# Optimization experiments

Hardware: AMD Instinct MI355X
Metric: run time of the kernel (lower is better)

The kernel has to match this reference:

```python
import jax, jax.numpy as jnp
import numpy as np
import math

B, T, O, C, H, L, V, S = 4, 1024, 128, 1024, 16, 4, 32000, 4096
D = C // H
PAD = 0


def setup_inputs() -> dict:
    key = jax.random.key(0)
    ks = jax.random.split(key, 16)
    r = lambda i, shape, s=0.02: jax.random.normal(ks[i], shape, jnp.float32) * s
    return {
        "tokens_w": jax.random.randint(ks[0], (B, T), 0, V).astype(jnp.int32),
        "pos_offset": 0,
        "mem": jax.random.normal(ks[1], (B, O, C), jnp.float32),
        "ssum": jax.random.normal(ks[2], (B, C), jnp.float32),
        "tok_emb_w": r(3, (V, C)),
        "pos_emb_w": r(4, (S, C)),
        "mem_w": r(5, (C, C)), "mem_b": jnp.zeros((C,), jnp.float32),
        "memln_s": jnp.ones((C,), jnp.float32), "memln_b": jnp.zeros((C,), jnp.float32),
        "alpha_p": jnp.zeros((C,), jnp.float32),
        "sum_w": r(6, (C, C)),
        "ln1_s": jnp.ones((L, C), jnp.float32), "ln1_b": jnp.zeros((L, C), jnp.float32),
        "Wq": r(7, (L, C, C)), "bq": jnp.zeros((L, C), jnp.float32),
        "Wk": r(8, (L, C, C)), "bk": jnp.zeros((L, C), jnp.float32),
        "Wv": r(9, (L, C, C)), "bv": jnp.zeros((L, C), jnp.float32),
        "Wo": r(10, (L, C, C)), "bo": jnp.zeros((L, C), jnp.float32),
        "ln2_s": jnp.ones((L, C), jnp.float32), "ln2_b": jnp.zeros((L, C), jnp.float32),
        "W1": r(11, (L, C, 4 * C)), "b1": jnp.zeros((L, 4 * C), jnp.float32),
        "W2": r(12, (L, 4 * C, C)), "b2": jnp.zeros((L, C), jnp.float32),
        "fln_s": jnp.ones((C,), jnp.float32), "fln_b": jnp.zeros((C,), jnp.float32),
        "head_w": r(13, (C, V)), "head_b": jnp.zeros((V,), jnp.float32),
        "lam_p": jnp.zeros((C,), jnp.float32),
    }


def _ln(x, s, b, eps=1e-6):
    mu = jnp.mean(x, -1, keepdims=True)
    var = jnp.mean((x - mu) ** 2, -1, keepdims=True)
    return (x - mu) * jax.lax.rsqrt(var + eps) * s + b


def reference(tokens_w, pos_offset, mem, ssum, tok_emb_w, pos_emb_w, mem_w, mem_b,
              memln_s, memln_b, alpha_p, sum_w, ln1_s, ln1_b, Wq, bq, Wk, bk, Wv, bv,
              Wo, bo, ln2_s, ln2_b, W1, b1, W2, b2, fln_s, fln_b, head_w, head_b, lam_p):
    Bx, Tx = tokens_w.shape
    tok = tok_emb_w[tokens_w]                                   # [B,T,C]
    pos_ids = jnp.clip(jnp.arange(Tx, dtype=jnp.int32) + pos_offset, 0, S - 1)
    x = tok + pos_emb_w[pos_ids][None, :, :]
    # memory adapter + norm (saved-before-masking memory state)
    m2 = _ln(mem @ mem_w + mem_b, memln_s, memln_b)             # [B,O,C]
    alpha = jax.nn.sigmoid(alpha_p)
    x = x + ((ssum @ sum_w) * alpha[None, :])[:, None, :]
    # boolean mask: memory tokens always visible + causal window + key padding
    causal = jnp.concatenate([jnp.ones((Tx, O), bool),
                              jnp.tril(jnp.ones((Tx, Tx), bool))], axis=1)[None, None]
    key_ok = jnp.concatenate([jnp.ones((Bx, O), bool), tokens_w != PAD], axis=1)
    mask = causal & key_ok[:, None, None, :]                    # [B,1,T,O+T]
    scale = 1.0 / math.sqrt(D)
    for i in range(L):
        kv = jnp.concatenate([m2, x], axis=1)                   # [B,O+T,C]
        h = _ln(x, ln1_s[i], ln1_b[i])
        q = (h @ Wq[i] + bq[i]).reshape(Bx, Tx, H, D)
        k = (kv @ Wk[i] + bk[i]).reshape(Bx, O + Tx, H, D)
        v = (kv @ Wv[i] + bv[i]).reshape(Bx, O + Tx, H, D)
        att = jnp.einsum('bqhd,bkhd->bhqk', q, k) * scale
        att = jnp.where(mask, att, -1e9)
        p = jax.nn.softmax(att, axis=-1)
        o = jnp.einsum('bhqk,bkhd->bqhd', p, v).reshape(Bx, Tx, C)
        x = x + (o @ Wo[i] + bo[i])
        h = _ln(x, ln2_s[i], ln2_b[i])
        x = x + (jax.nn.gelu(h @ W1[i] + b1[i]) @ W2[i] + b2[i])
    x = _ln(x, fln_s, fln_b)
    new_mem = x[:, -O:, :]
    m = (tokens_w != PAD).astype(x.dtype)
    x = x * m[:, :, None]
    logits = x @ head_w + head_b                                # [B,T,V]
    summary = jnp.sum(x * m[:, :, None], axis=1) / (jnp.sum(m, axis=1, keepdims=True) + 1e-6)
    lam = jax.nn.sigmoid(lam_p)
    new_ssum = ssum * lam[None, :] + summary * (1.0 - lam[None, :])
    return (new_mem, new_ssum, logits)
```

## Files before the change

### kernel.cpp

```cpp
#include <hip/hip_runtime.h>
#include <hip/hip_bf16.h>

typedef __bf16 bf16_t;
typedef __bf16 bf16x8 __attribute__((ext_vector_type(8)));
typedef __bf16 bf16x4 __attribute__((ext_vector_type(4)));
typedef float f32x4 __attribute__((ext_vector_type(4)));

#define NB 4
#define NT 1024
#define NO 128
#define NC 1024
#define NH 16
#define NL 4
#define NV 32000
#define NS 4096
#define ND 64
#define NTK (NO + NT)

#define GLOAD_LDS16(g, l) __builtin_amdgcn_global_load_lds( \
    (__attribute__((address_space(1))) void*)(g), \
    (__attribute__((address_space(3))) void*)(l), 16, 0, 0)

__device__ __forceinline__ float sigmoidf_(float x) { return 1.0f / (1.0f + __expf(-x)); }

template<int EPI>
__global__ __launch_bounds__(512) void gemm8p(
    const bf16_t* __restrict__ A, const bf16_t* __restrict__ Bt,
    const float* __restrict__ bias, float* __restrict__ outF,
    bf16_t* __restrict__ outB, int M, int N, int K, int ldo, int gm)
{
    __shared__ bf16_t sm[65536];
    const int tid = threadIdx.x;
    const int w = tid >> 6, lane = tid & 63;
    const int wr = w >> 2, wc = w & 3;
    const int lr = lane & 15, lk = lane >> 4;
    const int nwg = gridDim.x;
    const int bid = blockIdx.x;
    const int xcd = bid & 7, base = bid >> 3;
    const int qq = nwg >> 3, rr = nwg & 7;
    int wg = (xcd < rr ? xcd * (qq + 1) : rr * (qq + 1) + (xcd - rr) * qq) + base;
    const int nnt = N >> 8;
    const int gsz = gm * nnt;
    const int g = wg / gsz, r2 = wg - g * gsz;
    const int ntl = r2 / gm, mt = g * gm + (r2 - ntl * gm);
    const int bm = mt << 8, bn = ntl << 8;
    const bf16_t* Ab = A + (size_t)bm * K;
    const bf16_t* Bb = Bt + (size_t)bn * K;
    const int srow = tid >> 3;
    const int scol = ((tid & 7) ^ (srow & 7)) << 3;
    const int nk = K >> 6;
    f32x4 acc[8][4] = {};

    auto STAGE = [&](int b, int kt, int h) {
        const bf16_t* gsrc = (h < 2) ? Ab : Bb;
        const int half = h & 1;
        char* lbase = (char*)(sm + ((h < 2) ? 0 : 32768) + b * 16384 + half * 8192);
        #pragma unroll
        for (int i = 0; i < 2; ++i) {
            GLOAD_LDS16(gsrc + (size_t)(half * 128 + i * 64 + srow) * K + kt * 64 + scol,
                        lbase + (i * 512 + tid) * 16);
        }
    };

    #pragma unroll
    for (int h = 0; h < 4; ++h) STAGE(0, 0, h);
    asm volatile("s_waitcnt vmcnt(0)" ::: "memory");
    __builtin_amdgcn_s_barrier();

    for (int kt = 0; kt < nk; ++kt) {
        const int curb = kt & 1;
        const bool dostage = (kt + 1) < nk;
        const char* Abase = (const char*)(sm + curb * 16384);
        const char* Bbase = (const char*)(sm + 32768 + curb * 16384);

        if (dostage) {
            STAGE(curb ^ 1, kt + 1, 0);
            STAGE(curb ^ 1, kt + 1, 1);
            asm volatile("s_waitcnt vmcnt(4)" ::: "memory");
        } else {
            asm volatile("s_waitcnt vmcnt(0)" ::: "memory");
        }
        __builtin_amdgcn_s_barrier();

        bf16x8 bfr[4][2];
        #pragma unroll
        for (int n = 0; n < 4; ++n)
            #pragma unroll
            for (int ks = 0; ks < 2; ++ks) {
                const int row = wc * 64 + n * 16 + lr;
                bfr[n][ks] = *(const bf16x8*)(Bbase + row * 128 + ((((ks << 2) + lk) ^ (row & 7)) << 4));
            }
        bf16x8 af[4][2];
        #pragma unroll
        for (int m = 0; m < 4; ++m)
            #pragma unroll
            for (int ks = 0; ks < 2; ++ks) {
                const int row = wr * 128 + m * 16 + lr;
                af[m][ks] = *(const bf16x8*)(Abase + row * 128 + ((((ks << 2) + lk) ^ (row & 7)) << 4));
            }
        asm volatile("s_waitcnt lgkmcnt(0)" ::: "memory");
        __builtin_amdgcn_sched_barrier(0);
        __builtin_amdgcn_s_setprio(1);
        #pragma unroll
        for (int m = 0; m < 4; ++m)
            #pragma unroll
            for (int n = 0; n < 4; ++n)
                #pragma unroll
                for (int ks = 0; ks < 2; ++ks)
                    acc[m][n] = __builtin_amdgcn_mfma_f32_16x16x32_bf16(
                        af[m][ks], bfr[n][ks], acc[m][n], 0, 0, 0);
        __builtin_amdgcn_s_setprio(0);

        if (dostage) {
            STAGE(curb ^ 1, kt + 1, 2);
            STAGE(curb ^ 1, kt + 1, 3);
        }
        bf16x8 ag[4][2];
        #pragma unroll
        for (int m = 0; m < 4; ++m)
            #pragma unroll
            for (int ks = 0; ks < 2; ++ks) {
                const int row = wr * 128 + 64 + m * 16 + lr;
                ag[m][ks] = *(const bf16x8*)(Abase + row * 128 + ((((ks << 2) + lk) ^ (row & 7)) << 4));
            }
        asm volatile("s_waitcnt lgkmcnt(0)" ::: "memory");
        __builtin_amdgcn_sched_barrier(0);
        __builtin_amdgcn_s_setprio(1);
        #pragma unroll
        for (int m = 0; m < 4; ++m)
            #pragma unroll
            for (int n = 0; n < 4; ++n)
                #pragma unroll
                for (int ks = 0; ks < 2; ++ks)
                    acc[4 + m][n] = __builtin_amdgcn_mfma_f32_16x16x32_bf16(
                        ag[m][ks], bfr[n][ks], acc[4 + m][n], 0, 0, 0);
        __builtin_amdgcn_s_setprio(0);
        __builtin_amdgcn_s_barrier();
    }

    float bv4[4];
    #pragma unroll
    for (int n = 0; n < 4; ++n) bv4[n] = bias[bn + wc * 64 + n * 16 + lr];
    #pragma unroll
    for (int m = 0; m < 8; ++m) {
        #pragma unroll
        for (int j = 0; j < 4; ++j) {
            const int row = bm + wr * 128 + m * 16 + lk * 4 + j;
            #pragma unroll
            for (int n = 0; n < 4; ++n) {
                const int col = bn + wc * 64 + n * 16 + lr;
                float v = acc[m][n][j] + bv4[n];
                if constexpr (EPI == 0) {
                    __builtin_nontemporal_store(v, &outF[(size_t)row * ldo + col]);
                } else {
                    float u = 1.5957691216057308f * (v + 0.044715f * v * v * v);
                    float g_ = v / (1.0f + __expf(-u));
                    outB[(size_t)row * ldo + col] = (bf16_t)g_;
                }
            }
        }
    }
}

#define EPI_F32  0
#define EPI_ADD  1
#define EPI_GELU 2
#define EPI_QKV  3
#define EPI_KV   4

template<int EPI>
__global__ __launch_bounds__(256) void gemm_bt(
    const bf16_t* __restrict__ A, const bf16_t* __restrict__ Bt,
    const float* __restrict__ bias, const float* __restrict__ bias2,
    float* __restrict__ outF, bf16_t* __restrict__ outB, bf16_t* __restrict__ outB2,
    int M, int N, int K, int p0, int ldo, int gm)
{
    __shared__ bf16_t lA[128 * 32];
    __shared__ bf16_t lB[128 * 32];
    const int tid = threadIdx.x;
    const int nwg = gridDim.x;
    const int bid = blockIdx.x;
    const int xcd = bid & 7, base = bid >> 3;
    const int qq = nwg >> 3, rr = nwg & 7;
    int wg = (xcd < rr ? xcd * (qq + 1) : rr * (qq + 1) + (xcd - rr) * qq) + base;
    const int nnt = N >> 7;
    const int gsz = gm * nnt;
    const int g = wg / gsz, r2 = wg - g * gsz;
    const int ntl = r2 / gm, mt = g * gm + (r2 - ntl * gm);
    const int bm = mt * 128, bn = ntl * 128;
    const bf16_t* Ab = A + (size_t)bm * K;
    const bf16_t* Bb = Bt + (size_t)bn * K;
    const int wave = tid >> 6, lane = tid & 63;
    const int wr = wave >> 1, wc = wave & 1;
    const int lr = lane & 15, lk = lane >> 4;
    f32x4 acc[4][4] = {};
    const int nk = K >> 5;
    const int c1 = tid, c2 = tid + 256;
    for (int kt = 0; kt < nk; ++kt) {
        __syncthreads();
        const bf16_t* Abk = Ab + kt * 32;
        const bf16_t* Bbk = Bb + kt * 32;
        GLOAD_LDS16(Abk + (size_t)(c1 >> 2) * K + (c1 & 3) * 8, (char*)lA + c1 * 16);
        GLOAD_LDS16(Abk + (size_t)(c2 >> 2) * K + (c2 & 3) * 8, (char*)lA + c2 * 16);
        GLOAD_LDS16(Bbk + (size_t)(c1 >> 2) * K + (c1 & 3) * 8, (char*)lB + c1 * 16);
        GLOAD_LDS16(Bbk + (size_t)(c2 >> 2) * K + (c2 & 3) * 8, (char*)lB + c2 * 16);
        __syncthreads();
        bf16x8 af[4], bfr[4];
        #pragma unroll
        for (int m = 0; m < 4; ++m)
            af[m] = *(const bf16x8*)&lA[(wr * 64 + m * 16 + lr) * 32 + lk * 8];
        #pragma unroll
        for (int n = 0; n < 4; ++n)
            bfr[n] = *(const bf16x8*)&lB[(wc * 64 + n * 16 + lr) * 32 + lk * 8];
        #pragma unroll
        for (int m = 0; m < 4; ++m)
            #pragma unroll
            for (int n = 0; n < 4; ++n)
                acc[m][n] = __builtin_amdgcn_mfma_f32_16x16x32_bf16(af[m], bfr[n], acc[m][n], 0, 0, 0);
    }
    #pragma unroll
    for (int m = 0; m < 4; ++m) {
        #pragma unroll
        for (int j = 0; j < 4; ++j) {
            const int row = bm + wr * 64 + m * 16 + lk * 4 + j;
            int b_ = 0, t_ = 0;
            if constexpr (EPI == EPI_QKV || EPI == EPI_KV) { b_ = row / p0; t_ = row % p0; }
            #pragma unroll
            for (int n = 0; n < 4; ++n) {
                const int col = bn + wc * 64 + n * 16 + lr;
                if constexpr (EPI == EPI_F32) {
                    float v = acc[m][n][j] + bias[col];
                    __builtin_nontemporal_store(v, &outF[(size_t)row * ldo + col]);
                } else if constexpr (EPI == EPI_ADD) {
                    float v = acc[m][n][j] + bias[col];
                    outF[(size_t)row * ldo + col] += v;
                } else if constexpr (EPI == EPI_GELU) {
                    float v = acc[m][n][j] + bias[col];
                    float u = 1.5957691216057308f * (v + 0.044715f * v * v * v);
                    float g_ = v / (1.0f + __expf(-u));
                    outB[(size_t)row * ldo + col] = (bf16_t)g_;
                } else if constexpr (EPI == EPI_QKV) {
                    float v = acc[m][n][j] + bias[col];
                    int h = col >> 6, d = col & 63;
                    outB[(((size_t)b_ * NH + h) * p0 + t_) * ND + d] = (bf16_t)v;
                } else if constexpr (EPI == EPI_KV) {
                    if (col < NC) {
                        float v = acc[m][n][j] + bias[col];
                        int h = col >> 6, d = col & 63;
                        outB[(((size_t)b_ * NH + h) * NTK + t_) * ND + d] = (bf16_t)v;
                    } else {
                        int c2_ = col - NC;
                        float v = acc[m][n][j] + bias2[c2_];
                        int h = c2_ >> 6, d = c2_ & 63;
                        outB2[(((size_t)b_ * NH + h) * ND + d) * NTK + t_] = (bf16_t)v;
                    }
                }
            }
        }
    }
}

__device__ __forceinline__ void tc_body(
    const float* __restrict__ W, bf16_t* __restrict__ Wt,
    int K, int N, int k0, int n0, int t)
{
    __shared__ float tile[64][65];
    #pragma unroll
    for (int i = 0; i < 4; ++i) {
        const int idx = t + i * 256;
        const int r = idx >> 4, c4 = (idx & 15) << 2;
        const float4 v = *(const float4*)(W + (size_t)(k0 + r) * N + n0 + c4);
        tile[r][c4 + 0] = v.x; tile[r][c4 + 1] = v.y;
        tile[r][c4 + 2] = v.z; tile[r][c4 + 3] = v.w;
    }
    __syncthreads();
    #pragma unroll
    for (int i = 0; i < 4; ++i) {
        const int idx = t + i * 256;
        const int r = idx >> 4, c4 = (idx & 15) << 2;
        bf16x4 o = {(bf16_t)tile[c4 + 0][r], (bf16_t)tile[c4 + 1][r],
                    (bf16_t)tile[c4 + 2][r], (bf16_t)tile[c4 + 3][r]};
        *(bf16x4*)(Wt + (size_t)(n0 + r) * K + k0 + c4) = o;
    }
}

__global__ __launch_bounds__(256) void transpose_cast(
    const float* __restrict__ W, bf16_t* __restrict__ Wt, int K, int N)
{
    tc_body(W, Wt, K, N, blockIdx.x << 6, blockIdx.y << 6, threadIdx.x);
}

__global__ __launch_bounds__(256) void transpose_layer(
    const float* __restrict__ Wq, const float* __restrict__ Wk,
    const float* __restrict__ Wv, const float* __restrict__ Wo,
    const float* __restrict__ W1, const float* __restrict__ W2,
    bf16_t* __restrict__ wtq, bf16_t* __restrict__ wtkv,
    bf16_t* __restrict__ wto, bf16_t* __restrict__ wt1, bf16_t* __restrict__ wt2)
{
    const int bid = blockIdx.x;
    const float* W; bf16_t* Wt; int K, N, k0, n0;
    if (bid < 1024) {
        const int which = bid >> 8, r = bid & 255;
        K = NC; N = NC;
        k0 = (r & 15) << 6; n0 = (r >> 4) << 6;
        W  = (which == 0) ? Wq : (which == 1) ? Wk : (which == 2) ? Wv : Wo;
        Wt = (which == 0) ? wtq : (which == 1) ? wtkv
           : (which == 2) ? (wtkv + (size_t)NC * NC) : wto;
    } else if (bid < 2048) {
        const int r = bid - 1024;
        K = NC; N = 4 * NC;
        k0 = (r & 15) << 6; n0 = (r >> 4) << 6;
        W = W1; Wt = wt1;
    } else {
        const int r = bid - 2048;
        K = 4 * NC; N = NC;
        k0 = (r & 63) << 6; n0 = (r >> 6) << 6;
        W = W2; Wt = wt2;
    }
    tc_body(W, Wt, K, N, k0, n0, threadIdx.x);
}

template<int MODE>
__global__ __launch_bounds__(256) void ln_row(
    const float* __restrict__ X, const float* __restrict__ sw,
    const float* __restrict__ bw, float* __restrict__ outF,
    bf16_t* __restrict__ outB, bf16_t* __restrict__ outB2)
{
    const int row = blockIdx.x;
    const int t = threadIdx.x;
    const float4 v = ((const float4*)(X + (size_t)row * NC))[t];
    float s1 = v.x + v.y + v.z + v.w;
    float s2 = v.x * v.x + v.y * v.y + v.z * v.z + v.w * v.w;
    #pragma unroll
    for (int off = 32; off > 0; off >>= 1) { s1 += __shfl_xor(s1, off); s2 += __shfl_xor(s2, off); }
    __shared__ float rs1[4], rs2[4];
    if ((t & 63) == 0) { rs1[t >> 6] = s1; rs2[t >> 6] = s2; }
    __syncthreads();
    s1 = rs1[0] + rs1[1] + rs1[2] + rs1[3];
    s2 = rs2[0] + rs2[1] + rs2[2] + rs2[3];
    const float mu = s1 * (1.0f / NC);
    const float var = s2 * (1.0f / NC) - mu * mu;
    const float rstd = rsqrtf(var + 1e-6f);
    const int c = t * 4;
    const float4 sv = ((const float4*)sw)[t];
    const float4 bv = ((const float4*)bw)[t];
    float y0 = (v.x - mu) * rstd * sv.x + bv.x;
    float y1 = (v.y - mu) * rstd * sv.y + bv.y;
    float y2 = (v.z - mu) * rstd * sv.z + bv.z;
    float y3 = (v.w - mu) * rstd * sv.w + bv.w;
    size_t dst;
    if constexpr (MODE == 1) dst = ((size_t)(row / NO) * NTK + (row % NO)) * NC + c;
    else dst = (size_t)row * NC + c;
    bf16x4 o = {(bf16_t)y0, (bf16_t)y1, (bf16_t)y2, (bf16_t)y3};
    *(bf16x4*)(outB + dst) = o;
    if constexpr (MODE == 3) {
        const int b_ = row >> 10, t_ = row & 1023;
        bf16x4 o2 = {(bf16_t)v.x, (bf16_t)v.y, (bf16_t)v.z, (bf16_t)v.w};
        *(bf16x4*)(outB2 + ((size_t)b_ * NTK + NO + t_) * NC + c) = o2;
    }
}

__global__ __launch_bounds__(256) void ln_final(
    const float* __restrict__ X, const float* __restrict__ sw,
    const float* __restrict__ bw, const int* __restrict__ tokens,
    bf16_t* __restrict__ xm, float* __restrict__ outMem)
{
    const int row = blockIdx.x;
    const int t = threadIdx.x;
    const float4 v = ((const float4*)(X + (size_t)row * NC))[t];
    float s1 = v.x + v.y + v.z + v.w;
    float s2 = v.x * v.x + v.y * v.y + v.z * v.z + v.w * v.w;
    #pragma unroll
    for (int off = 32; off > 0; off >>= 1) { s1 += __shfl_xor(s1, off); s2 += __shfl_xor(s2, off); }
    __shared__ float rs1[4], rs2[4];
    if ((t & 63) == 0) { rs1[t >> 6] = s1; rs2[t >> 6] = s2; }
    __syncthreads();
    s1 = rs1[0] + rs1[1] + rs1[2] + rs1[3];
    s2 = rs2[0] + rs2[1] + rs2[2] + rs2[3];
    const float mu = s1 * (1.0f / NC);
    const float var = s2 * (1.0f / NC) - mu * mu;
    const float rstd = rsqrtf(var + 1e-6f);
    const int c = t * 4;
    const float4 sv = ((const float4*)sw)[t];
    const float4 bv = ((const float4*)bw)[t];
    float y0 = (v.x - mu) * rstd * sv.x + bv.x;
    float y1 = (v.y - mu) * rstd * sv.y + bv.y;
    float y2 = (v.z - mu) * rstd * sv.z + bv.z;
    float y3 = (v.w - mu) * rstd * sv.w + bv.w;
    const bool ok = tokens[row] != 0;
    bf16x4 o;
    if (ok) { o = (bf16x4){(bf16_t)y0, (bf16_t)y1, (bf16_t)y2, (bf16_t)y3}; }
    else    { o = (bf16x4){(bf16_t)0.f, (bf16_t)0.f, (bf16_t)0.f, (bf16_t)0.f}; }
    *(bf16x4*)(xm + (size_t)row * NC + c) = o;
    const int b_ = row >> 10, t_ = row & 1023;
    if (t_ >= NT - NO) {
        float4 f; f.x = y0; f.y = y1; f.z = y2; f.w = y3;
        *(float4*)(outMem + ((size_t)b_ * NO + (t_ - (NT - NO))) * NC + c) = f;
    }
}

__global__ __launch_bounds__(256) void attn_kernel(
    const bf16_t* __restrict__ Q, const bf16_t* __restrict__ Kb,
    const bf16_t* __restrict__ Vt, const int* __restrict__ tokens,
    bf16_t* __restrict__ Ob)
{
    const int bh = blockIdx.x;
    const int b = bh >> 4, h = bh & 15;
    const int w = threadIdx.x >> 6;
    const int lane = threadIdx.x & 63;
    const int yt = gridDim.y - 1 - blockIdx.y;
    const int q0 = (yt << 6) + (w << 4);
    const int lr = lane & 15, lk = lane >> 4;
    const bf16_t* Qp = Q + ((size_t)bh * NT + q0) * ND;
    const bf16x8 qf0 = *(const bf16x8*)(Qp + lr * ND + lk * 8);
    const bf16x8 qf1 = *(const bf16x8*)(Qp + lr * ND + 32 + lk * 8);
    const bf16_t* Kbase = Kb + (size_t)bh * NTK * ND;
    const bf16_t* Vbase = Vt + (size_t)bh * ND * NTK;
    const int* tokb = tokens + b * NT;
    float mrow[4] = {-1e30f, -1e30f, -1e30f, -1e30f};
    float lsum[4] = {0.f, 0.f, 0.f, 0.f};
    f32x4 acc[4] = {};
    __shared__ bf16_t pb[4][16 * 64];
    char* pbw = (char*)pb[w];
    const int kmax = NO + q0 + 16;
    for (int k0 = 0; k0 < kmax; k0 += 64) {
        f32x4 st[4] = {};
        __builtin_amdgcn_s_setprio(1);
        #pragma unroll
        for (int nt = 0; nt < 4; ++nt) {
            const bf16_t* Kp = Kbase + (size_t)(k0 + nt * 16 + lr) * ND + lk * 8;
            bf16x8 kf0 = *(const bf16x8*)(Kp);
            bf16x8 kf1 = *(const bf16x8*)(Kp + 32);
            st[nt] = __builtin_amdgcn_mfma_f32_16x16x32_bf16(qf0, kf0, st[nt], 0, 0, 0);
            st[nt] = __builtin_amdgcn_mfma_f32_16x16x32_bf16(qf1, kf1, st[nt], 0, 0, 0);
        }
        __builtin_amdgcn_s_setprio(0);
        float sc[4][4];
        float tmax[4] = {-1e30f, -1e30f, -1e30f, -1e30f};
        #pragma unroll
        for (int nt = 0; nt < 4; ++nt) {
            const int key = k0 + nt * 16 + lr;
            const int kt = key - NO;
            const int kts = kt < 0 ? 0 : kt;
            const bool keyok = (kt < 0) | (tokb[kts] != 0);
            #pragma unroll
            for (int j = 0; j < 4; ++j) {
                const int qrow = q0 + lk * 4 + j;
                const bool ok = keyok && (kt <= qrow);
                const float s = ok ? st[nt][j] * 0.125f : -1e9f;
                sc[nt][j] = s;
                tmax[j] = fmaxf(tmax[j], s);
            }
        }
        #pragma unroll
        for (int off = 1; off < 16; off <<= 1)
            #pragma unroll
            for (int j = 0; j < 4; ++j) tmax[j] = fmaxf(tmax[j], __shfl_xor(tmax[j], off));
        float resc[4], p[4][4], psum[4] = {0.f, 0.f, 0.f, 0.f};
        #pragma unroll
        for (int j = 0; j < 4; ++j) {
            const float mnew = fmaxf(mrow[j], tmax[j]);
            resc[j] = __expf(mrow[j] - mnew);
            mrow[j] = mnew;
        }
        #pragma unroll
        for (int nt = 0; nt < 4; ++nt)
            #pragma unroll
            for (int j = 0; j < 4; ++j) { p[nt][j] = __expf(sc[nt][j] - mrow[j]); psum[j] += p[nt][j]; }
        #pragma unroll
        for (int off = 1; off < 16; off <<= 1)
            #pragma unroll
            for (int j = 0; j < 4; ++j) psum[j] += __shfl_xor(psum[j], off);
        #pragma unroll
        for (int j = 0; j < 4; ++j) lsum[j] = lsum[j] * resc[j] + psum[j];
        #pragma unroll
        for (int dt = 0; dt < 4; ++dt)
            #pragma unroll
            for (int j = 0; j < 4; ++j) acc[dt][j] *= resc[j];
        #pragma unroll
        for (int nt = 0; nt < 4; ++nt)
            #pragma unroll
            for (int j = 0; j < 4; ++j) {
                const int row = lk * 4 + j;
                const int byt = (row << 7) + ((((nt << 4) + lr) << 1) ^ ((row & 7) << 4));
                *(bf16_t*)(pbw + byt) = (bf16_t)p[nt][j];
            }
        const int swz = (lr & 7) << 4;
        const bf16x8 pa0 = *(const bf16x8*)(pbw + ((lr << 7) + (((lk << 4)) ^ swz)));
        const bf16x8 pa1 = *(const bf16x8*)(pbw + ((lr << 7) + ((64 + (lk << 4)) ^ swz)));
        __builtin_amdgcn_s_setprio(1);
        #pragma unroll
        for (int dt = 0; dt < 4; ++dt) {
            const bf16_t* Vp = Vbase + (size_t)(dt * 16 + lr) * NTK + k0 + lk * 8;
            bf16x8 vf0 = *(const bf16x8*)(Vp);
            bf16x8 vf1 = *(const bf16x8*)(Vp + 32);
            acc[dt] = __builtin_amdgcn_mfma_f32_16x16x32_bf16(pa0, vf0, acc[dt], 0, 0, 0);
            acc[dt] = __builtin_amdgcn_mfma_f32_16x16x32_bf16(pa1, vf1, acc[dt], 0, 0, 0);
        }
        __builtin_amdgcn_s_setprio(0);
    }
    #pragma unroll
    for (int dt = 0; dt < 4; ++dt)
        #pragma unroll
        for (int j = 0; j < 4; ++j)
            Ob[((size_t)b * NT + q0 + lk * 4 + j) * NC + h * ND + dt * 16 + lr] =
                (bf16_t)(acc[dt][j] / lsum[j]);
}

__global__ __launch_bounds__(256) void sum_proj_kernel(
    const float* __restrict__ ssum, const float* __restrict__ sumw,
    const float* __restrict__ alpha, float* __restrict__ add)
{
    const int b = blockIdx.y;
    const int c = blockIdx.x * 256 + threadIdx.x;
    float a = 0.f;
    for (int k = 0; k < NC; ++k) a += ssum[b * NC + k] * sumw[(size_t)k * NC + c];
    add[b * NC + c] = a * sigmoidf_(alpha[c]);
}

__global__ __launch_bounds__(256) void embed_kernel(
    const int* __restrict__ tokens, const int* __restrict__ posoff,
    const float* __restrict__ tokw, const float* __restrict__ posw,
    const float* __restrict__ add, float* __restrict__ X)
{
    const int bt = blockIdx.x;
    const int b = bt >> 10, t = bt & 1023;
    const int c = threadIdx.x * 4;
    const int tok = tokens[bt];
    int p = t + posoff[0];
    p = p < 0 ? 0 : (p > NS - 1 ? NS - 1 : p);
    const float4 tv = *(const float4*)(tokw + (size_t)tok * NC + c);
    const float4 pv = *(const float4*)(posw + (size_t)p * NC + c);
    const float4 av = *(const float4*)(add + b * NC + c);
    float4 o;
    o.x = tv.x + pv.x + av.x; o.y = tv.y + pv.y + av.y;
    o.z = tv.z + pv.z + av.z; o.w = tv.w + pv.w + av.w;
    *(float4*)(X + (size_t)bt * NC + c) = o;
}

__global__ __launch_bounds__(256) void cast_f32_bf16_kernel(
    const float* __restrict__ in, bf16_t* __restrict__ out)
{
    const size_t i = ((size_t)blockIdx.x * 256 + threadIdx.x) * 4;
    const float4 v = *(const float4*)(in + i);
    bf16x4 o = {(bf16_t)v.x, (bf16_t)v.y, (bf16_t)v.z, (bf16_t)v.w};
    *(bf16x4*)(out + i) = o;
}

__global__ __launch_bounds__(256) void sumpart_kernel(
    const bf16_t* __restrict__ XM, float* __restrict__ sbuf)
{
    const int b = blockIdx.z;
    const int c = blockIdx.x * 256 + threadIdx.x;
    const int t0 = blockIdx.y * 64;
    float a = 0.f;
    for (int t = t0; t < t0 + 64; ++t)
        a += (float)XM[((size_t)b * NT + t) * NC + c];
    atomicAdd(&sbuf[b * NC + c], a);
}

__global__ __launch_bounds__(256) void ssum_out_kernel(
    const float* __restrict__ sbuf, const int* __restrict__ tokens,
    const float* __restrict__ ssum, const float* __restrict__ lamp, float* __restrict__ out)
{
    const int b = blockIdx.y;
    const int c = blockIdx.x * 256 + threadIdx.x;
    int cnt = 0;
    for (int t = 0; t < NT; ++t) cnt += (tokens[b * NT + t] != 0);
    const float summary = sbuf[b * NC + c] / ((float)cnt + 1e-6f);
    const float lam = sigmoidf_(lamp[c]);
    out[b * NC + c] = ssum[b * NC + c] * lam + summary * (1.0f - lam);
}

extern "C" void kernel_launch(void* const* d_in, const int* in_sizes, int n_in,
                              void* d_out, int out_size, void* d_ws, size_t ws_size,
                              hipStream_t stream)
{
    (void)in_sizes; (void)n_in; (void)out_size; (void)ws_size;
    const int*   tokens   = (const int*)d_in[0];
    const int*   posoff   = (const int*)d_in[1];
    const float* mem      = (const float*)d_in[2];
    const float* ssum     = (const float*)d_in[3];
    const float* tok_emb  = (const float*)d_in[4];
    const float* pos_emb  = (const float*)d_in[5];
    const float* mem_w    = (const float*)d_in[6];
    const float* mem_b    = (const float*)d_in[7];
    const float* memln_s  = (const float*)d_in[8];
    const float* memln_b  = (const float*)d_in[9];
    const float* alpha_p  = (const float*)d_in[10];
    const float* sum_w    = (const float*)d_in[11];
    const float* ln1_s    = (const float*)d_in[12];
    const float* ln1_b    = (const float*)d_in[13];
    const float* Wq       = (const float*)d_in[14];
    const float* bq       = (const float*)d_in[15];
    const float* Wk       = (const float*)d_in[16];
    const float* bk       = (const float*)d_in[17];
    const float* Wv       = (const float*)d_in[18];
    const float* bv       = (const float*)d_in[19];
    const float* Wo       = (const float*)d_in[20];
    const float* bo       = (const float*)d_in[21];
    const float* ln2_s    = (const float*)d_in[22];
    const float* ln2_b    = (const float*)d_in[23];
    const float* W1       = (const float*)d_in[24];
    const float* b1       = (const float*)d_in[25];
    const float* W2       = (const float*)d_in[26];
    const float* b2       = (const float*)d_in[27];
    const float* fln_s    = (const float*)d_in[28];
    const float* fln_b    = (const float*)d_in[29];
    const float* head_w   = (const float*)d_in[30];
    const float* head_b   = (const float*)d_in[31];
    const float* lam_p    = (const float*)d_in[32];

    float* out_mem    = (float*)d_out;
    float* out_ssum   = out_mem + (size_t)NB * NO * NC;
    float* out_logits = out_ssum + (size_t)NB * NC;

    char* wp = (char*)d_ws;
    auto alloc = [&](size_t bytes) { char* p = wp; wp += (bytes + 255) & ~(size_t)255; return p; };
    bf16_t* wt_head = (bf16_t*)alloc((size_t)NV * NC * 2);
    bf16_t* wt_mem  = (bf16_t*)alloc((size_t)NC * NC * 2);
    bf16_t* wt_q    = (bf16_t*)alloc((size_t)NC * NC * 2);
    bf16_t* wt_kv   = (bf16_t*)alloc((size_t)2 * NC * NC * 2);
    bf16_t* wt_o    = (bf16_t*)alloc((size_t)NC * NC * 2);
    bf16_t* wt_1    = (bf16_t*)alloc((size_t)NC * 4 * NC * 2);
    bf16_t* wt_2    = (bf16_t*)alloc((size_t)NC * 4 * NC * 2);
    float*  xbuf    = (float*)alloc((size_t)NB * NT * NC * 4);
    bf16_t* hbuf    = (bf16_t*)alloc((size_t)NB * NT * NC * 2);
    bf16_t* kvbuf   = (bf16_t*)alloc((size_t)NB * NTK * NC * 2);
    bf16_t* qbuf    = (bf16_t*)alloc((size_t)NB * NT * NC * 2);
    bf16_t* kbuf    = (bf16_t*)alloc((size_t)NB * NTK * NC * 2);
    bf16_t* vtbuf   = (bf16_t*)alloc((size_t)NB * NTK * NC * 2);
    bf16_t* obuf    = (bf16_t*)alloc((size_t)NB * NT * NC * 2);
    bf16_t* midbuf  = (bf16_t*)alloc((size_t)NB * NT * 4 * NC * 2);
    bf16_t* xmbuf   = (bf16_t*)alloc((size_t)NB * NT * NC * 2);
    bf16_t* membf   = (bf16_t*)alloc((size_t)NB * NO * NC * 2);
    float*  m2f     = (float*)alloc((size_t)NB * NO * NC * 4);
    float*  addb    = (float*)alloc((size_t)NB * NC * 4);
    float*  sbuf    = (float*)alloc((size_t)NB * NC * 4);

    hipMemsetAsync(sbuf, 0, (size_t)NB * NC * 4, stream);

    transpose_cast<<<dim3(NC / 64, NV / 64), 256, 0, stream>>>(head_w, wt_head, NC, NV);
    transpose_cast<<<dim3(NC / 64, NC / 64), 256, 0, stream>>>(mem_w, wt_mem, NC, NC);

    cast_f32_bf16_kernel<<<(NB * NO * NC) / 1024, 256, 0, stream>>>(mem, membf);
    gemm_bt<EPI_F32><<<32, 256, 0, stream>>>(
        membf, wt_mem, mem_b, nullptr, m2f, nullptr, nullptr, NB * NO, NC, NC, 0, NC, 4);
    ln_row<1><<<NB * NO, 256, 0, stream>>>(m2f, memln_s, memln_b, nullptr, kvbuf, nullptr);

    sum_proj_kernel<<<dim3(NC / 256, NB), 256, 0, stream>>>(ssum, sum_w, alpha_p, addb);
    embed_kernel<<<NB * NT, 256, 0, stream>>>(tokens, posoff, tok_emb, pos_emb, addb, xbuf);

    for (int i = 0; i < NL; ++i) {
        transpose_layer<<<3072, 256, 0, stream>>>(
            Wq + (size_t)i * NC * NC, Wk + (size_t)i * NC * NC,
            Wv + (size_t)i * NC * NC, Wo + (size_t)i * NC * NC,
            W1 + (size_t)i * NC * 4 * NC, W2 + (size_t)i * 4 * NC * NC,
            wt_q, wt_kv, wt_o, wt_1, wt_2);

        ln_row<3><<<NB * NT, 256, 0, stream>>>(xbuf, ln1_s + i * NC, ln1_b + i * NC, nullptr, hbuf, kvbuf);

        gemm_bt<EPI_QKV><<<256, 256, 0, stream>>>(
            hbuf, wt_q, bq + i * NC, nullptr, nullptr, qbuf, nullptr, NB * NT, NC, NC, NT, 0, 8);
        gemm_bt<EPI_KV><<<576, 256, 0, stream>>>(
            kvbuf, wt_kv, bk + i * NC, bv + i * NC, nullptr, kbuf, vtbuf, NB * NTK, 2 * NC, NC, NTK, 0, 6);

        attn_kernel<<<dim3(NB * NH, NT / 64), 256, 0, stream>>>(qbuf, kbuf, vtbuf, tokens, obuf);

        gemm_bt<EPI_ADD><<<256, 256, 0, stream>>>(
            obuf, wt_o, bo + i * NC, nullptr, xbuf, nullptr, nullptr, NB * NT, NC, NC, 0, NC, 8);

        ln_row<0><<<NB * NT, 256, 0, stream>>>(xbuf, ln2_s + i * NC, ln2_b + i * NC, nullptr, hbuf, nullptr);
        gemm8p<1><<<256, 512, 0, stream>>>(
            hbuf, wt_1, b1 + (size_t)i * 4 * NC, nullptr, midbuf, NB * NT, 4 * NC, NC, 4 * NC, 4);
        gemm_bt<EPI_ADD><<<256, 256, 0, stream>>>(
            midbuf, wt_2, b2 + i * NC, nullptr, xbuf, nullptr, nullptr, NB * NT, NC, 4 * NC, 0, NC, 8);
    }

    ln_final<<<NB * NT, 256, 0, stream>>>(xbuf, fln_s, fln_b, tokens, xmbuf, out_mem);
    sumpart_kernel<<<dim3(NC / 256, NT / 64, NB), 256, 0, stream>>>(xmbuf, sbuf);
    ssum_out_kernel<<<dim3(NC / 256, NB), 256, 0, stream>>>(sbuf, tokens, ssum, lam_p, out_ssum);
    gemm8p<0><<<2000, 512, 0, stream>>>(
        xmbuf, wt_head, head_b, out_logits, nullptr, NB * NT, NV, NC, NV, 4);
}
```

Baseline: 1.919 ms.

## Add double-buffered swizzled LDS GEMM and widen attention to 32 query rows per wave

Adds a new 128x128 GEMM kernel that streams A and B tiles into LDS with direct global-to-LDS loads, a 64-deep K step, XOR swizzling and double buffering. Tile loads for the next step overlap with the MFMAs of the current one. It replaces the older single-buffered gemm_bt for the QKV, KV, output and FFN-down projections, and the FFN-down grouping drops from 8 to 2. The attention kernel now handles two 16-row query subtiles per wave, so each K/V fragment load serves twice the MFMAs, at the cost of more registers and half as many blocks.

```diff
diff --git a/kernel.cpp b/kernel.cpp
--- a/kernel.cpp
+++ b/kernel.cpp
@@ -22,6 +22,12 @@
     (__attribute__((address_space(3))) void*)(l), 16, 0, 0)
 
 __device__ __forceinline__ float sigmoidf_(float x) { return 1.0f / (1.0f + __expf(-x)); }
+
+#define EPI_F32  0
+#define EPI_ADD  1
+#define EPI_GELU 2
+#define EPI_QKV  3
+#define EPI_KV   4
 
 template<int EPI>
 __global__ __launch_bounds__(512) void gemm8p(
@@ -162,11 +168,145 @@
     }
 }
 
-#define EPI_F32  0
-#define EPI_ADD  1
-#define EPI_GELU 2
-#define EPI_QKV  3
-#define EPI_KV   4
+template<int EPI>
+__global__ __launch_bounds__(256) void gemm128(
+    const bf16_t* __restrict__ A, const bf16_t* __restrict__ Bt,
+    const float* __restrict__ bias, const float* __restrict__ bias2,
+    float* __restrict__ outF, bf16_t* __restrict__ outB, bf16_t* __restrict__ outB2,
+    int M, int N, int K, int p0, int ldo, int gm)
+{
+    __shared__ bf16_t sm[32768];
+    char* smb = (char*)sm;
+    const int tid = threadIdx.x;
+    const int w = tid >> 6, lane = tid & 63;
+    const int wr = w >> 1, wc = w & 1;
+    const int lr = lane & 15, lk = lane >> 4;
+    const int nwg = gridDim.x;
+    const int bid = blockIdx.x;
+    const int xcd = bid & 7, base = bid >> 3;
+    const int qq = nwg >> 3, rr = nwg & 7;
+    int wg = (xcd < rr ? xcd * (qq + 1) : rr * (qq + 1) + (xcd - rr) * qq) + base;
+    const int nnt = N >> 7;
+    const int gsz = gm * nnt;
+    const int g = wg / gsz, r2 = wg - g * gsz;
+    const int ntl = r2 / gm, mt = g * gm + (r2 - ntl * gm);
+    const int bm = mt << 7, bn = ntl << 7;
+    const bf16_t* Ab = A + (size_t)bm * K;
+    const bf16_t* Bb = Bt + (size_t)bn * K;
+    const int srow = tid >> 3;
+    const int scol = ((tid & 7) ^ (srow & 7)) << 3;
+    const int nk = K >> 6;
+    f32x4 acc[4][4] = {};
+
+    auto STAGE = [&](int b, int kt, int h) {
+        const bf16_t* gsrc = h ? Bb : Ab;
+        char* lbase = smb + h * 32768 + b * 16384;
+        #pragma unroll
+        for (int i = 0; i < 4; ++i) {
+            GLOAD_LDS16(gsrc + (size_t)(i * 32 + srow) * K + kt * 64 + scol,
+                        lbase + (i * 256 + tid) * 16);
+        }
+    };
+
+    STAGE(0, 0, 0); STAGE(0, 0, 1);
+    asm volatile("s_waitcnt vmcnt(0)" ::: "memory");
+    __builtin_amdgcn_s_barrier();
+
+    for (int kt = 0; kt < nk; ++kt) {
+        const int curb = kt & 1;
+        const bool dostage = (kt + 1) < nk;
+        const char* Abase = smb + curb * 16384;
+        const char* Bbase = smb + 32768 + curb * 16384;
+
+        if (dostage) {
+            STAGE(curb ^ 1, kt + 1, 0);
+            asm volatile("s_waitcnt vmcnt(4)" ::: "memory");
+        } else {
+            asm volatile("s_waitcnt vmcnt(0)" ::: "memory");
+        }
+        __builtin_amdgcn_s_barrier();
+
+        bf16x8 bfr[4][2];
+        #pragma unroll
+        for (int n = 0; n < 4; ++n)
+            #pragma unroll
+            for (int ks = 0; ks < 2; ++ks) {
+                const int row = wc * 64 + n * 16 + lr;
+                bfr[n][ks] = *(const bf16x8*)(Bbase + row * 128 + ((((ks << 2) + lk) ^ (row & 7)) << 4));
+            }
+        bf16x8 af[4];
+        #pragma unroll
+        for (int m = 0; m < 4; ++m) {
+            const int row = wr * 64 + m * 16 + lr;
+            af[m] = *(const bf16x8*)(Abase + row * 128 + (((lk) ^ (row & 7)) << 4));
+        }
+        asm volatile("s_waitcnt lgkmcnt(0)" ::: "memory");
+        __builtin_amdgcn_sched_barrier(0);
+        __builtin_amdgcn_s_setprio(1);
+        #pragma unroll
+        for (int m = 0; m < 4; ++m)
+            #pragma unroll
+            for (int n = 0; n < 4; ++n)
+                acc[m][n] = __builtin_amdgcn_mfma_f32_16x16x32_bf16(
+                    af[m], bfr[n][0], acc[m][n], 0, 0, 0);
+        __builtin_amdgcn_s_setprio(0);
+
+        if (dostage) STAGE(curb ^ 1, kt + 1, 1);
+        bf16x8 ag[4];
+        #pragma unroll
+        for (int m = 0; m < 4; ++m) {
+            const int row = wr * 64 + m * 16 + lr;
+            ag[m] = *(const bf16x8*)(Abase + row * 128 + (((4 + lk) ^ (row & 7)) << 4));
+        }
+        asm volatile("s_waitcnt lgkmcnt(0)" ::: "memory");
+        __builtin_amdgcn_sched_barrier(0);
+        __builtin_amdgcn_s_setprio(1);
+        #pragma unroll
+        for (int m = 0; m < 4; ++m)
+            #pragma unroll
+            for (int n = 0; n < 4; ++n)
+                acc[m][n] = __builtin_amdgcn_mfma_f32_16x16x32_bf16(
+                    ag[m], bfr[n][1], acc[m][n], 0, 0, 0);
+        __builtin_amdgcn_s_setprio(0);
+        __builtin_amdgcn_s_barrier();
+    }
+
+    #pragma unroll
+    for (int m = 0; m < 4; ++m) {
+        #pragma unroll
+        for (int j = 0; j < 4; ++j) {
+            const int row = bm + wr * 64 + m * 16 + lk * 4 + j;
+            int b_ = 0, t_ = 0;
+            if constexpr (EPI == EPI_QKV || EPI == EPI_KV) { b_ = row / p0; t_ = row % p0; }
+            #pragma unroll
+            for (int n = 0; n < 4; ++n) {
+                const int col = bn + wc * 64 + n * 16 + lr;
+                if constexpr (EPI == EPI_F32) {
+                    float v = acc[m][n][j] + bias[col];
+                    __builtin_nontemporal_store(v, &outF[(size_t)row * ldo + col]);
+                } else if constexpr (EPI == EPI_ADD) {
+                    float v = acc[m][n][j] + bias[col];
+                    outF[(size_t)row * ldo + col] += v;
+                } else if constexpr (EPI == EPI_QKV) {
+                    float v = acc[m][n][j] + bias[col];
+                    int h = col >> 6, d = col & 63;
+                    outB[(((size_t)b_ * NH + h) * p0 + t_) * ND + d] = (bf16_t)v;
+                } else if constexpr (EPI == EPI_KV) {
+                    if (col < NC) {
+                        float v = acc[m][n][j] + bias[col];
+                        int h = col >> 6, d = col & 63;
+                        outB[(((size_t)b_ * NH + h) * NTK + t_) * ND + d] = (bf16_t)v;
+                    } else {
+                        int c2_ = col - NC;
+                        float v = acc[m][n][j] + bias2[c2_];
+                        int h = c2_ >> 6, d = c2_ & 63;
+                        outB2[(((size_t)b_ * NH + h) * ND + d) * NTK + t_] = (bf16_t)v;
+                    }
+                }
+            }
+        }
+    }
+}
 
 template<int EPI>
 __global__ __launch_bounds__(256) void gemm_bt(
@@ -223,37 +363,12 @@
         #pragma unroll
         for (int j = 0; j < 4; ++j) {
             const int row = bm + wr * 64 + m * 16 + lk * 4 + j;
-            int b_ = 0, t_ = 0;
-            if constexpr (EPI == EPI_QKV || EPI == EPI_KV) { b_ = row / p0; t_ = row % p0; }
             #pragma unroll
             for (int n = 0; n < 4; ++n) {
                 const int col = bn + wc * 64 + n * 16 + lr;
                 if constexpr (EPI == EPI_F32) {
                     float v = acc[m][n][j] + bias[col];
                     __builtin_nontemporal_store(v, &outF[(size_t)row * ldo + col]);
-                } else if constexpr (EPI == EPI_ADD) {
-                    float v = acc[m][n][j] + bias[col];
-                    outF[(size_t)row * ldo + col] += v;
-                } else if constexpr (EPI == EPI_GELU) {
-                    float v = acc[m][n][j] + bias[col];
-                    float u = 1.5957691216057308f * (v + 0.044715f * v * v * v);
-                    float g_ = v / (1.0f + __expf(-u));
-                    outB[(size_t)row * ldo + col] = (bf16_t)g_;
-                } else if constexpr (EPI == EPI_QKV) {
-                    float v = acc[m][n][j] + bias[col];
-                    int h = col >> 6, d = col & 63;
-                    outB[(((size_t)b_ * NH + h) * p0 + t_) * ND + d] = (bf16_t)v;
-                } else if constexpr (EPI == EPI_KV) {
-                    if (col < NC) {
-                        float v = acc[m][n][j] + bias[col];
-                        int h = col >> 6, d = col & 63;
-                        outB[(((size_t)b_ * NH + h) * NTK + t_) * ND + d] = (bf16_t)v;
-                    } else {
-                        int c2_ = col - NC;
-                        float v = acc[m][n][j] + bias2[c2_];
-                        int h = c2_ >> 6, d = c2_ & 63;
-                        outB2[(((size_t)b_ * NH + h) * ND + d) * NTK + t_] = (bf16_t)v;
-                    }
                 }
             }
         }
@@ -409,102 +524,122 @@
     const int w = threadIdx.x >> 6;
     const int lane = threadIdx.x & 63;
     const int yt = gridDim.y - 1 - blockIdx.y;
-    const int q0 = (yt << 6) + (w << 4);
+    const int q0 = (yt << 7) + (w << 5);
     const int lr = lane & 15, lk = lane >> 4;
     const bf16_t* Qp = Q + ((size_t)bh * NT + q0) * ND;
-    const bf16x8 qf0 = *(const bf16x8*)(Qp + lr * ND + lk * 8);
-    const bf16x8 qf1 = *(const bf16x8*)(Qp + lr * ND + 32 + lk * 8);
+    bf16x8 qf[2][2];
+    #pragma unroll
+    for (int qs = 0; qs < 2; ++qs) {
+        qf[qs][0] = *(const bf16x8*)(Qp + (qs * 16 + lr) * ND + lk * 8);
+        qf[qs][1] = *(const bf16x8*)(Qp + (qs * 16 + lr) * ND + 32 + lk * 8);
+    }
     const bf16_t* Kbase = Kb + (size_t)bh * NTK * ND;
     const bf16_t* Vbase = Vt + (size_t)bh * ND * NTK;
     const int* tokb = tokens + b * NT;
-    float mrow[4] = {-1e30f, -1e30f, -1e30f, -1e30f};
-    float lsum[4] = {0.f, 0.f, 0.f, 0.f};
-    f32x4 acc[4] = {};
-    __shared__ bf16_t pb[4][16 * 64];
-    char* pbw = (char*)pb[w];
-    const int kmax = NO + q0 + 16;
+    float mrow[2][4] = {{-1e30f, -1e30f, -1e30f, -1e30f}, {-1e30f, -1e30f, -1e30f, -1e30f}};
+    float lsum[2][4] = {};
+    f32x4 acc[2][4] = {};
+    __shared__ bf16_t pb[4][2][16 * 64];
+    const int kmax = NO + q0 + 32;
     for (int k0 = 0; k0 < kmax; k0 += 64) {
-        f32x4 st[4] = {};
+        f32x4 st[2][4] = {};
         __builtin_amdgcn_s_setprio(1);
         #pragma unroll
         for (int nt = 0; nt < 4; ++nt) {
             const bf16_t* Kp = Kbase + (size_t)(k0 + nt * 16 + lr) * ND + lk * 8;
             bf16x8 kf0 = *(const bf16x8*)(Kp);
             bf16x8 kf1 = *(const bf16x8*)(Kp + 32);
-            st[nt] = __builtin_amdgcn_mfma_f32_16x16x32_bf16(qf0, kf0, st[nt], 0, 0, 0);
-            st[nt] = __builtin_amdgcn_mfma_f32_16x16x32_bf16(qf1, kf1, st[nt], 0, 0, 0);
+            #pragma unroll
+            for (int qs = 0; qs < 2; ++qs) {
+                st[qs][nt] = __builtin_amdgcn_mfma_f32_16x16x32_bf16(qf[qs][0], kf0, st[qs][nt], 0, 0, 0);
+                st[qs][nt] = __builtin_amdgcn_mfma_f32_16x16x32_bf16(qf[qs][1], kf1, st[qs][nt], 0, 0, 0);
+            }
         }
         __builtin_amdgcn_s_setprio(0);
-        float sc[4][4];
-        float tmax[4] = {-1e30f, -1e30f, -1e30f, -1e30f};
-        #pragma unroll
-        for (int nt = 0; nt < 4; ++nt) {
-            const int key = k0 + nt * 16 + lr;
-            const int kt = key - NO;
-            const int kts = kt < 0 ? 0 : kt;
-            const bool keyok = (kt < 0) | (tokb[kts] != 0);
+        #pragma unroll
+        for (int qs = 0; qs < 2; ++qs) {
+            char* pbq = (char*)pb[w][qs];
+            float sc[4][4];
+            float tmax[4] = {-1e30f, -1e30f, -1e30f, -1e30f};
+            #pragma unroll
+            for (int nt = 0; nt < 4; ++nt) {
+                const int key = k0 + nt * 16 + lr;
+                const int kt = key - NO;
+                const int kts = kt < 0 ? 0 : kt;
+                const bool keyok = (kt < 0) | (tokb[kts] != 0);
+                #pragma unroll
+                for (int j = 0; j < 4; ++j) {
+                    const int qrow = q0 + qs * 16 + lk * 4 + j;
+                    const bool ok = keyok && (kt <= qrow);
+                    const float s = ok ? st[qs][nt][j] * 0.125f : -1e9f;
+                    sc[nt][j] = s;
+                    tmax[j] = fmaxf(tmax[j], s);
+                }
+            }
+            #pragma unroll
+            for (int off = 1; off < 16; off <<= 1)
+                #pragma unroll
+                for (int j = 0; j < 4; ++j) tmax[j] = fmaxf(tmax[j], __shfl_xor(tmax[j], off));
+            float resc[4], p[4][4], psum[4] = {0.f, 0.f, 0.f, 0.f};
             #pragma unroll
             for (int j = 0; j < 4; ++j) {
-                const int qrow = q0 + lk * 4 + j;
-                const bool ok = keyok && (kt <= qrow);
-                const float s = ok ? st[nt][j] * 0.125f : -1e9f;
-                sc[nt][j] = s;
-                tmax[j] = fmaxf(tmax[j], s);
-            }
-        }
-        #pragma unroll
-        for (int off = 1; off < 16; off <<= 1)
-            #pragma unroll
-            for (int j = 0; j < 4; ++j) tmax[j] = fmaxf(tmax[j], __shfl_xor(tmax[j], off));
-        float resc[4], p[4][4], psum[4] = {0.f, 0.f, 0.f, 0.f};
-        #pragma unroll
-        for (int j = 0; j < 4; ++j) {
-            const float mnew = fmaxf(mrow[j], tmax[j]);
-            resc[j] = __expf(mrow[j] - mnew);
-            mrow[j] = mnew;
-        }
-        #pragma unroll
-        for (int nt = 0; nt < 4; ++nt)
-            #pragma unroll
-            for (int j = 0; j < 4; ++j) { p[nt][j] = __expf(sc[nt][j] - mrow[j]); psum[j] += p[nt][j]; }
-        #pragma unroll
-        for (int off = 1; off < 16; off <<= 1)
-            #pragma unroll
-            for (int j = 0; j < 4; ++j) psum[j] += __shfl_xor(psum[j], off);
-        #pragma unroll
-        for (int j = 0; j < 4; ++j) lsum[j] = lsum[j] * resc[j] + psum[j];
-        #pragma unroll
-        for (int dt = 0; dt < 4; ++dt)
-            #pragma unroll
-            for (int j = 0; j < 4; ++j) acc[dt][j] *= resc[j];
-        #pragma unroll
-        for (int nt = 0; nt < 4; ++nt)
-            #pragma unroll
-            for (int j = 0; j < 4; ++j) {
-                const int row = lk * 4 + j;
-                const int byt = (row << 7) + ((((nt << 4) + lr) << 1) ^ ((row & 7) << 4));
-                *(bf16_t*)(pbw + byt) = (bf16_t)p[nt][j];
-            }
+                const float mnew = fmaxf(mrow[qs][j], tmax[j]);
+                resc[j] = __expf(mrow[qs][j] - mnew);
+                mrow[qs][j] = mnew;
+            }
+            #pragma unroll
+            for (int nt = 0; nt < 4; ++nt)
+                #pragma unroll
+                for (int j = 0; j < 4; ++j) { p[nt][j] = __expf(sc[nt][j] - mrow[qs][j]); psum[j] += p[nt][j]; }
+            #pragma unroll
+            for (int off = 1; off < 16; off <<= 1)
+                #pragma unroll
+                for (int j = 0; j < 4; ++j) psum[j] += __shfl_xor(psum[j], off);
+            #pragma unroll
+            for (int j = 0; j < 4; ++j) lsum[qs][j] = lsum[qs][j] * resc[j] + psum[j];
+            #pragma unroll
+            for (int dt = 0; dt < 4; ++dt)
+                #pragma unroll
+                for (int j = 0; j < 4; ++j) acc[qs][dt][j] *= resc[j];
+            #pragma unroll
+            for (int nt = 0; nt < 4; ++nt)
+                #pragma unroll
+                for (int j = 0; j < 4; ++j) {
+                    const int row = lk * 4 + j;
+                    const int byt = (row << 7) + ((((nt << 4) + lr) << 1) ^ ((row & 7) << 4));
+                    *(bf16_t*)(pbq + byt) = (bf16_t)p[nt][j];
+                }
+        }
         const int swz = (lr & 7) << 4;
-        const bf16x8 pa0 = *(const bf16x8*)(pbw + ((lr << 7) + (((lk << 4)) ^ swz)));
-        const bf16x8 pa1 = *(const bf16x8*)(pbw + ((lr << 7) + ((64 + (lk << 4)) ^ swz)));
+        bf16x8 pa[2][2];
+        #pragma unroll
+        for (int qs = 0; qs < 2; ++qs) {
+            const char* pbq = (const char*)pb[w][qs];
+            pa[qs][0] = *(const bf16x8*)(pbq + ((lr << 7) + (((lk << 4)) ^ swz)));
+            pa[qs][1] = *(const bf16x8*)(pbq + ((lr << 7) + ((64 + (lk << 4)) ^ swz)));
+        }
         __builtin_amdgcn_s_setprio(1);
         #pragma unroll
         for (int dt = 0; dt < 4; ++dt) {
             const bf16_t* Vp = Vbase + (size_t)(dt * 16 + lr) * NTK + k0 + lk * 8;
             bf16x8 vf0 = *(const bf16x8*)(Vp);
             bf16x8 vf1 = *(const bf16x8*)(Vp + 32);
-            acc[dt] = __builtin_amdgcn_mfma_f32_16x16x32_bf16(pa0, vf0, acc[dt], 0, 0, 0);
-            acc[dt] = __builtin_amdgcn_mfma_f32_16x16x32_bf16(pa1, vf1, acc[dt], 0, 0, 0);
+            #pragma unroll
+            for (int qs = 0; qs < 2; ++qs) {
+                acc[qs][dt] = __builtin_amdgcn_mfma_f32_16x16x32_bf16(pa[qs][0], vf0, acc[qs][dt], 0, 0, 0);
+                acc[qs][dt] = __builtin_amdgcn_mfma_f32_16x16x32_bf16(pa[qs][1], vf1, acc[qs][dt], 0, 0, 0);
+            }
         }
         __builtin_amdgcn_s_setprio(0);
     }
     #pragma unroll
-    for (int dt = 0; dt < 4; ++dt)
-        #pragma unroll
-        for (int j = 0; j < 4; ++j)
-            Ob[((size_t)b * NT + q0 + lk * 4 + j) * NC + h * ND + dt * 16 + lr] =
-                (bf16_t)(acc[dt][j] / lsum[j]);
+    for (int qs = 0; qs < 2; ++qs)
+        #pragma unroll
+        for (int dt = 0; dt < 4; ++dt)
+            #pragma unroll
+            for (int j = 0; j < 4; ++j)
+                Ob[((size_t)b * NT + q0 + qs * 16 + lk * 4 + j) * NC + h * ND + dt * 16 + lr] =
+                    (bf16_t)(acc[qs][dt][j] / lsum[qs][j]);
 }
 
 __global__ __launch_bounds__(256) void sum_proj_kernel(
@@ -660,21 +795,21 @@
 
         ln_row<3><<<NB * NT, 256, 0, stream>>>(xbuf, ln1_s + i * NC, ln1_b + i * NC, nullptr, hbuf, kvbuf);
 
-        gemm_bt<EPI_QKV><<<256, 256, 0, stream>>>(
+        gemm128<EPI_QKV><<<256, 256, 0, stream>>>(
             hbuf, wt_q, bq + i * NC, nullptr, nullptr, qbuf, nullptr, NB * NT, NC, NC, NT, 0, 8);
-        gemm_bt<EPI_KV><<<576, 256, 0, stream>>>(
+        gemm128<EPI_KV><<<576, 256, 0, stream>>>(
             kvbuf, wt_kv, bk + i * NC, bv + i * NC, nullptr, kbuf, vtbuf, NB * NTK, 2 * NC, NC, NTK, 0, 6);
 
-        attn_kernel<<<dim3(NB * NH, NT / 64), 256, 0, stream>>>(qbuf, kbuf, vtbuf, tokens, obuf);
-
-        gemm_bt<EPI_ADD><<<256, 256, 0, stream>>>(
+        attn_kernel<<<dim3(NB * NH, NT / 128), 256, 0, stream>>>(qbuf, kbuf, vtbuf, tokens, obuf);
+
+        gemm128<EPI_ADD><<<256, 256, 0, stream>>>(
             obuf, wt_o, bo + i * NC, nullptr, xbuf, nullptr, nullptr, NB * NT, NC, NC, 0, NC, 8);
 
         ln_row<0><<<NB * NT, 256, 0, stream>>>(xbuf, ln2_s + i * NC, ln2_b + i * NC, nullptr, hbuf, nullptr);
         gemm8p<1><<<256, 512, 0, stream>>>(
             hbuf, wt_1, b1 + (size_t)i * 4 * NC, nullptr, midbuf, NB * NT, 4 * NC, NC, 4 * NC, 4);
-        gemm_bt<EPI_ADD><<<256, 256, 0, stream>>>(
-            midbuf, wt_2, b2 + i * NC, nullptr, xbuf, nullptr, nullptr, NB * NT, NC, 4 * NC, 0, NC, 8);
+        gemm128<EPI_ADD><<<256, 256, 0, stream>>>(
+            midbuf, wt_2, b2 + i * NC, nullptr, xbuf, nullptr, nullptr, NB * NT, NC, 4 * NC, 0, NC, 2);
     }
 
     ln_final<<<NB * NT, 256, 0, stream>>>(xbuf, fln_s, fln_b, tokens, xmbuf, out_mem);
```

Measured after the change: 1.723 ms. -10.3%, faster.
